# Performance work log

Measured on AMD Instinct MI355X. Metric: run time of the kernel, lower is better.

## Reference

```python
import jax, jax.numpy as jnp
import numpy as np

ANCHOR_NUM = 8
CLASS_NUM = 2
IN_DIM = 1024

def setup_inputs() -> dict:
    key = jax.random.key(0)
    k1, k2, k3, k4 = jax.random.split(key, 4)
    batch_input = jax.random.normal(k1, (64, 512, IN_DIM), dtype=jnp.float32)
    # labels in {-1, 0, 1}: -1 = padding, 0 = negative anchor, 1 = positive anchor
    anchor_labels = jax.random.randint(k2, (64, 512, ANCHOR_NUM), 0, 3, dtype=jnp.int64 if jax.config.read('jax_enable_x64') else jnp.int32) - 1
    lim = 1.0 / np.sqrt(IN_DIM)
    W = jax.random.uniform(k3, (IN_DIM, ANCHOR_NUM * CLASS_NUM), dtype=jnp.float32, minval=-lim, maxval=lim)
    b = jax.random.uniform(k4, (ANCHOR_NUM * CLASS_NUM,), dtype=jnp.float32, minval=-lim, maxval=lim)
    return {"batch_input": batch_input, "W": W, "b": b, "anchor_labels": anchor_labels}

def reference(batch_input, W, b, anchor_labels):
    B, S, _ = batch_input.shape
    # logits: (B, S, anchor_num, class_num)
    logits = (jnp.einsum('bsd,dk->bsk', batch_input, W) + b).reshape(B, S, ANCHOR_NUM, CLASS_NUM)
    predict_label = jnp.argmax(logits, axis=3)  # (B, S, A)
    valid = (anchor_labels != -1)
    labels = jnp.maximum(anchor_labels, 0)  # safe class index for padded entries
    logp = jax.nn.log_softmax(logits, axis=-1)
    nll = -jnp.take_along_axis(logp, labels[..., None].astype(jnp.int32), axis=-1)[..., 0]
    # CrossEntropyLoss (mean) over all non-padding anchors == eval-path gather + CE
    vf = valid.astype(logits.dtype)
    loss = jnp.sum(nll * vf) / jnp.maximum(jnp.sum(vf), 1.0)
    # candidate mask stands in for candidate_idx (positive predictions, non-padding)
    candidate_mask = (predict_label == 1) & valid
    return loss, predict_label, candidate_mask
```

## Files before the change

kernel.cpp:

```cpp
#include <hip/hip_runtime.h>
#include <math.h>


#define ROWS   64
#define NW     8
#define KSLICE 128
#define KCH    16
#define NCH    (KSLICE/KCH)
#define RSTR   136

__global__ __launch_bounds__(512, 2)
void rpn_main(const float* __restrict__ x, const float* __restrict__ W,
              const float* __restrict__ b, const int* __restrict__ lab,
              float* __restrict__ out, float* __restrict__ ws)
{
    __shared__ float red[ROWS * RSTR];

    const int tid  = threadIdx.x;
    const int lane = tid & 63;
    const int ks   = __builtin_amdgcn_readfirstlane(tid >> 6);
    const int row0 = blockIdx.x * ROWS;

    const float* xp = x + (size_t)(row0 + lane) * 1024 + ks * KSLICE;
    const float* wk = W + (size_t)(ks * KSLICE) * 16;

    float acc[16];
#pragma unroll
    for (int c = 0; c < 16; ++c) acc[c] = 0.f;

    float4 pf[4];
#pragma unroll
    for (int j = 0; j < 4; ++j) pf[j] = *(const float4*)(xp + j * 4);

#define FMA16(V, WROW)                                            \
    do {                                                          \
        const float* _w = (WROW);                                 \
        _Pragma("unroll")                                         \
        for (int c = 0; c < 16; ++c)                              \
            acc[c] = fmaf((V), _w[c], acc[c]);                    \
    } while (0)

#pragma unroll 1
    for (int ch = 0; ch < NCH - 1; ++ch) {
        const float* wc = wk + ch * KCH * 16;
        const float* gn = xp + (ch + 1) * KCH;
#pragma unroll
        for (int j = 0; j < 4; ++j) {
            float4 v = pf[j];
            pf[j] = *(const float4*)(gn + j * 4);
            FMA16(v.x, wc + (j * 4 + 0) * 16);
            FMA16(v.y, wc + (j * 4 + 1) * 16);
            FMA16(v.z, wc + (j * 4 + 2) * 16);
            FMA16(v.w, wc + (j * 4 + 3) * 16);
        }
    }
    {
        const float* wc = wk + (NCH - 1) * KCH * 16;
#pragma unroll
        for (int j = 0; j < 4; ++j) {
            float4 v = pf[j];
            FMA16(v.x, wc + (j * 4 + 0) * 16);
            FMA16(v.y, wc + (j * 4 + 1) * 16);
            FMA16(v.z, wc + (j * 4 + 2) * 16);
            FMA16(v.w, wc + (j * 4 + 3) * 16);
        }
    }
#undef FMA16

    __syncthreads();
    {
        float* rp = red + lane * RSTR + ks * 16;
        *(float4*)(rp + 0)  = make_float4(acc[0],  acc[1],  acc[2],  acc[3]);
        *(float4*)(rp + 4)  = make_float4(acc[4],  acc[5],  acc[6],  acc[7]);
        *(float4*)(rp + 8)  = make_float4(acc[8],  acc[9],  acc[10], acc[11]);
        *(float4*)(rp + 12) = make_float4(acc[12], acc[13], acc[14], acc[15]);
    }
    __syncthreads();

    if (tid < ROWS) {
        const int row = row0 + tid;
        float L[16];
#pragma unroll
        for (int c = 0; c < 16; ++c) {
            float s = 0.f;
#pragma unroll
            for (int k = 0; k < NW; ++k) s += red[tid * RSTR + k * 16 + c];
            L[c] = s + b[c];
        }

        const int* labp  = lab + (size_t)row * 8;
        float*     predp = out + 1 + (size_t)row * 8;
        float*     maskp = out + 1 + 262144 + (size_t)row * 8;

        float lsum = 0.f, lcnt = 0.f;
#pragma unroll
        for (int a = 0; a < 8; ++a) {
            float l0 = L[2 * a], l1 = L[2 * a + 1];
            int   lb = labp[a];
            int   pred  = (l1 > l0) ? 1 : 0;
            int   valid = (lb != -1);
            float m   = fmaxf(l0, l1);
            float lse = m + logf(expf(l0 - m) + expf(l1 - m));
            float nll = lse - ((lb == 1) ? l1 : l0);
            if (valid) { lsum += nll; lcnt += 1.f; }
            predp[a] = (float)pred;
            maskp[a] = (pred && valid) ? 1.f : 0.f;
        }

#pragma unroll
        for (int off = 32; off > 0; off >>= 1) {
            lsum += __shfl_down(lsum, off, 64);
            lcnt += __shfl_down(lcnt, off, 64);
        }
        if (tid == 0) {
            atomicAdd(&ws[0], lsum);
            atomicAdd(&ws[1], lcnt);
        }
    }
}

__global__ void rpn_final(const float* __restrict__ ws, float* __restrict__ out)
{
    out[0] = ws[0] / fmaxf(ws[1], 1.f);
}

extern "C" void kernel_launch(void* const* d_in, const int* in_sizes, int n_in,
                              void* d_out, int out_size, void* d_ws, size_t ws_size,
                              hipStream_t stream)
{
    const float* x   = (const float*)d_in[0];
    const float* W   = (const float*)d_in[1];
    const float* b   = (const float*)d_in[2];
    const int*   lab = (const int*)d_in[3];
    float* out = (float*)d_out;
    float* ws  = (float*)d_ws;

    hipMemsetAsync(ws, 0, 2 * sizeof(float), stream);
    rpn_main<<<dim3(512), dim3(512), 0, stream>>>(x, W, b, lab, out, ws);
    rpn_final<<<dim3(1), dim3(1), 0, stream>>>(ws, out);
}
```

Measured before the change: 211.8 us.

## Stage x tiles into LDS via global_load_lds with swizzled layout

```diff
diff --git a/kernel.cpp b/kernel.cpp
--- a/kernel.cpp
+++ b/kernel.cpp
@@ -5,32 +5,46 @@
 #define ROWS   64
 #define NW     8
 #define KSLICE 128
-#define KCH    16
-#define NCH    (KSLICE/KCH)
+#define CHUNK  32
+#define NCH    (KSLICE/CHUNK)
+#define SLABF  (ROWS*CHUNK)
 #define RSTR   136
+
+typedef __attribute__((address_space(3))) void       lds_v;
+typedef const __attribute__((address_space(1))) void gbl_v;
+
+__device__ __forceinline__ void stage16(const float* g, float* l)
+{
+    __builtin_amdgcn_global_load_lds((gbl_v*)g, (lds_v*)l, 16, 0, 0);
+}
 
 __global__ __launch_bounds__(512, 2)
 void rpn_main(const float* __restrict__ x, const float* __restrict__ W,
               const float* __restrict__ b, const int* __restrict__ lab,
               float* __restrict__ out, float* __restrict__ ws)
 {
-    __shared__ float red[ROWS * RSTR];
+    __shared__ float xs[NW * SLABF];
+    float* red = xs;
 
     const int tid  = threadIdx.x;
     const int lane = tid & 63;
     const int ks   = __builtin_amdgcn_readfirstlane(tid >> 6);
     const int row0 = blockIdx.x * ROWS;
 
-    const float* xp = x + (size_t)(row0 + lane) * 1024 + ks * KSLICE;
-    const float* wk = W + (size_t)(ks * KSLICE) * 16;
+    const int rsub = lane >> 3;
+    const int tq   = (lane & 7) ^ rsub;
+
+    float* slab = xs + ks * SLABF;
+    const float* gstage = x + (size_t)(row0 + rsub) * 1024 + ks * KSLICE + tq * 4;
+    const float* wk     = W + (size_t)(ks * KSLICE) * 16;
 
     float acc[16];
 #pragma unroll
     for (int c = 0; c < 16; ++c) acc[c] = 0.f;
 
-    float4 pf[4];
 #pragma unroll
-    for (int j = 0; j < 4; ++j) pf[j] = *(const float4*)(xp + j * 4);
+    for (int i = 0; i < 8; ++i)
+        stage16(gstage + i * 8192, slab + i * 256);
 
 #define FMA16(V, WROW)                                            \
     do {                                                          \
@@ -41,28 +55,31 @@
     } while (0)
 
 #pragma unroll 1
-    for (int ch = 0; ch < NCH - 1; ++ch) {
-        const float* wc = wk + ch * KCH * 16;
-        const float* gn = xp + (ch + 1) * KCH;
+    for (int ch = 0; ch < NCH; ++ch) {
+        asm volatile("s_waitcnt vmcnt(0)" ::: "memory");
+        __builtin_amdgcn_sched_barrier(0);
+
+        float4 xq[8];
 #pragma unroll
-        for (int j = 0; j < 4; ++j) {
-            float4 v = pf[j];
-            pf[j] = *(const float4*)(gn + j * 4);
-            FMA16(v.x, wc + (j * 4 + 0) * 16);
-            FMA16(v.y, wc + (j * 4 + 1) * 16);
-            FMA16(v.z, wc + (j * 4 + 2) * 16);
-            FMA16(v.w, wc + (j * 4 + 3) * 16);
+        for (int t = 0; t < 8; ++t)
+            xq[t] = *(const float4*)(slab + lane * 32 + ((t ^ (lane & 7)) << 2));
+
+        asm volatile("s_waitcnt lgkmcnt(0)" ::: "memory");
+        __builtin_amdgcn_sched_barrier(0);
+        if (ch + 1 < NCH) {
+            const float* g = gstage + (ch + 1) * CHUNK;
+#pragma unroll
+            for (int i = 0; i < 8; ++i)
+                stage16(g + i * 8192, slab + i * 256);
         }
-    }
-    {
-        const float* wc = wk + (NCH - 1) * KCH * 16;
+
+        const float* wc = wk + (size_t)(ch * CHUNK) * 16;
 #pragma unroll
-        for (int j = 0; j < 4; ++j) {
-            float4 v = pf[j];
-            FMA16(v.x, wc + (j * 4 + 0) * 16);
-            FMA16(v.y, wc + (j * 4 + 1) * 16);
-            FMA16(v.z, wc + (j * 4 + 2) * 16);
-            FMA16(v.w, wc + (j * 4 + 3) * 16);
+        for (int t = 0; t < 8; ++t) {
+            FMA16(xq[t].x, wc + (t * 4 + 0) * 16);
+            FMA16(xq[t].y, wc + (t * 4 + 1) * 16);
+            FMA16(xq[t].z, wc + (t * 4 + 2) * 16);
+            FMA16(xq[t].w, wc + (t * 4 + 3) * 16);
         }
     }
 #undef FMA16
```

Result: no change. 215.7 us (+1.9%).

## Split K across two blocks per row tile and move epilogue to final kernel

Applied to the files above, without the earlier changes.

```diff
diff --git a/kernel.cpp b/kernel.cpp
--- a/kernel.cpp
+++ b/kernel.cpp
@@ -4,25 +4,29 @@
 
 #define ROWS   64
 #define NW     8
-#define KSLICE 128
+#define KSL    64
 #define KCH    16
-#define NCH    (KSLICE/KCH)
-#define RSTR   136
+#define NCH    4
+#define RSTR   132
+#define PART_STRIDE (32768u * 16u)
 
-__global__ __launch_bounds__(512, 2)
+__global__ __launch_bounds__(512, 4)
 void rpn_main(const float* __restrict__ x, const float* __restrict__ W,
-              const float* __restrict__ b, const int* __restrict__ lab,
-              float* __restrict__ out, float* __restrict__ ws)
+              float* __restrict__ ws)
 {
     __shared__ float red[ROWS * RSTR];
 
     const int tid  = threadIdx.x;
     const int lane = tid & 63;
-    const int ks   = __builtin_amdgcn_readfirstlane(tid >> 6);
-    const int row0 = blockIdx.x * ROWS;
+    const int wv   = __builtin_amdgcn_readfirstlane(tid >> 6);
+    const int rb   = blockIdx.x & 511;
+    const int kb   = blockIdx.x >> 9;
+    const int row0 = rb * ROWS;
+    const int kse  = (wv + blockIdx.x) & 7;
+    const int chr  = (blockIdx.x >> 3) & 3;
 
-    const float* xp = x + (size_t)(row0 + lane) * 1024 + ks * KSLICE;
-    const float* wk = W + (size_t)(ks * KSLICE) * 16;
+    const float* xp = x + (size_t)(row0 + lane) * 1024 + kb * 512 + kse * KSL;
+    const float* wk = W + (size_t)(kb * 512 + kse * KSL) * 16;
 
     float acc[16];
 #pragma unroll
@@ -30,7 +34,8 @@
 
     float4 pf[4];
 #pragma unroll
-    for (int j = 0; j < 4; ++j) pf[j] = *(const float4*)(xp + j * 4);
+    for (int j = 0; j < 4; ++j)
+        pf[j] = *(const float4*)(xp + chr * KCH + j * 4);
 
 #define FMA16(V, WROW)                                            \
     do {                                                          \
@@ -40,25 +45,16 @@
             acc[c] = fmaf((V), _w[c], acc[c]);                    \
     } while (0)
 
-#pragma unroll 1
-    for (int ch = 0; ch < NCH - 1; ++ch) {
-        const float* wc = wk + ch * KCH * 16;
-        const float* gn = xp + (ch + 1) * KCH;
+#pragma unroll
+    for (int ci = 0; ci < NCH; ++ci) {
+        const int ch  = (ci + chr) & 3;
+        const int chn = (ci + 1 + chr) & 3;
+        const float* wc = wk + ch * (KCH * 16);
 #pragma unroll
         for (int j = 0; j < 4; ++j) {
             float4 v = pf[j];
-            pf[j] = *(const float4*)(gn + j * 4);
-            FMA16(v.x, wc + (j * 4 + 0) * 16);
-            FMA16(v.y, wc + (j * 4 + 1) * 16);
-            FMA16(v.z, wc + (j * 4 + 2) * 16);
-            FMA16(v.w, wc + (j * 4 + 3) * 16);
-        }
-    }
-    {
-        const float* wc = wk + (NCH - 1) * KCH * 16;
-#pragma unroll
-        for (int j = 0; j < 4; ++j) {
-            float4 v = pf[j];
+            if (ci != NCH - 1)
+                pf[j] = *(const float4*)(xp + chn * KCH + j * 4);
             FMA16(v.x, wc + (j * 4 + 0) * 16);
             FMA16(v.y, wc + (j * 4 + 1) * 16);
             FMA16(v.z, wc + (j * 4 + 2) * 16);
@@ -69,7 +65,7 @@
 
     __syncthreads();
     {
-        float* rp = red + lane * RSTR + ks * 16;
+        float* rp = red + lane * RSTR + wv * 16;
         *(float4*)(rp + 0)  = make_float4(acc[0],  acc[1],  acc[2],  acc[3]);
         *(float4*)(rp + 4)  = make_float4(acc[4],  acc[5],  acc[6],  acc[7]);
         *(float4*)(rp + 8)  = make_float4(acc[8],  acc[9],  acc[10], acc[11]);
@@ -77,51 +73,90 @@
     }
     __syncthreads();
 
-    if (tid < ROWS) {
-        const int row = row0 + tid;
-        float L[16];
+    if (tid < 256) {
+        const int row = tid >> 2;
+        const int c0  = (tid & 3) * 4;
+        float4 s = make_float4(0.f, 0.f, 0.f, 0.f);
 #pragma unroll
-        for (int c = 0; c < 16; ++c) {
-            float s = 0.f;
-#pragma unroll
-            for (int k = 0; k < NW; ++k) s += red[tid * RSTR + k * 16 + c];
-            L[c] = s + b[c];
+        for (int k = 0; k < NW; ++k) {
+            float4 t = *(const float4*)(red + row * RSTR + k * 16 + c0);
+            s.x += t.x; s.y += t.y; s.z += t.z; s.w += t.w;
         }
-
-        const int* labp  = lab + (size_t)row * 8;
-        float*     predp = out + 1 + (size_t)row * 8;
-        float*     maskp = out + 1 + 262144 + (size_t)row * 8;
-
-        float lsum = 0.f, lcnt = 0.f;
-#pragma unroll
-        for (int a = 0; a < 8; ++a) {
-            float l0 = L[2 * a], l1 = L[2 * a + 1];
-            int   lb = labp[a];
-            int   pred  = (l1 > l0) ? 1 : 0;
-            int   valid = (lb != -1);
-            float m   = fmaxf(l0, l1);
-            float lse = m + logf(expf(l0 - m) + expf(l1 - m));
-            float nll = lse - ((lb == 1) ? l1 : l0);
-            if (valid) { lsum += nll; lcnt += 1.f; }
-            predp[a] = (float)pred;
-            maskp[a] = (pred && valid) ? 1.f : 0.f;
-        }
-
-#pragma unroll
-        for (int off = 32; off > 0; off >>= 1) {
-            lsum += __shfl_down(lsum, off, 64);
-            lcnt += __shfl_down(lcnt, off, 64);
-        }
-        if (tid == 0) {
-            atomicAdd(&ws[0], lsum);
-            atomicAdd(&ws[1], lcnt);
-        }
+        float* dst = ws + 8 + (size_t)kb * PART_STRIDE
+                   + (size_t)(row0 + row) * 16 + c0;
+        *(float4*)dst = s;
     }
 }
 
-__global__ void rpn_final(const float* __restrict__ ws, float* __restrict__ out)
+__global__ __launch_bounds__(256, 4)
+void rpn_final(const float* __restrict__ b, const int* __restrict__ lab,
+               float* __restrict__ out, float* __restrict__ ws)
 {
-    out[0] = ws[0] / fmaxf(ws[1], 1.f);
+    __shared__ float rsum[8];
+    const int tid = threadIdx.x;
+    const int row = blockIdx.x * 256 + tid;
+
+    const float* p0 = ws + 8 + (size_t)row * 16;
+    const float* p1 = p0 + PART_STRIDE;
+
+    float L[16];
+#pragma unroll
+    for (int q = 0; q < 4; ++q) {
+        float4 a0 = *(const float4*)(p0 + q * 4);
+        float4 a1 = *(const float4*)(p1 + q * 4);
+        L[q * 4 + 0] = a0.x + a1.x + b[q * 4 + 0];
+        L[q * 4 + 1] = a0.y + a1.y + b[q * 4 + 1];
+        L[q * 4 + 2] = a0.z + a1.z + b[q * 4 + 2];
+        L[q * 4 + 3] = a0.w + a1.w + b[q * 4 + 3];
+    }
+
+    const int* labp = lab + (size_t)row * 8;
+    float pv[8], mv[8];
+    float lsum = 0.f, lcnt = 0.f;
+#pragma unroll
+    for (int a = 0; a < 8; ++a) {
+        float l0 = L[2 * a], l1 = L[2 * a + 1];
+        int   lb = labp[a];
+        int   pred  = (l1 > l0) ? 1 : 0;
+        int   valid = (lb != -1);
+        float m   = fmaxf(l0, l1);
+        float lse = m + logf(expf(l0 - m) + expf(l1 - m));
+        float nll = lse - ((lb == 1) ? l1 : l0);
+        if (valid) { lsum += nll; lcnt += 1.f; }
+        pv[a] = (float)pred;
+        mv[a] = (pred && valid) ? 1.f : 0.f;
+    }
+
+    float* predp = out + 1 + (size_t)row * 8;
+    float* maskp = out + 1 + 262144 + (size_t)row * 8;
+    *(float4*)(predp)     = make_float4(pv[0], pv[1], pv[2], pv[3]);
+    *(float4*)(predp + 4) = make_float4(pv[4], pv[5], pv[6], pv[7]);
+    *(float4*)(maskp)     = make_float4(mv[0], mv[1], mv[2], mv[3]);
+    *(float4*)(maskp + 4) = make_float4(mv[4], mv[5], mv[6], mv[7]);
+
+#pragma unroll
+    for (int off = 32; off > 0; off >>= 1) {
+        lsum += __shfl_down(lsum, off, 64);
+        lcnt += __shfl_down(lcnt, off, 64);
+    }
+    if ((tid & 63) == 0) {
+        rsum[(tid >> 6) * 2]     = lsum;
+        rsum[(tid >> 6) * 2 + 1] = lcnt;
+    }
+    __syncthreads();
+    if (tid == 0) {
+        float S = rsum[0] + rsum[2] + rsum[4] + rsum[6];
+        float C = rsum[1] + rsum[3] + rsum[5] + rsum[7];
+        atomicAdd(&ws[0], S);
+        atomicAdd(&ws[1], C);
+        __threadfence();
+        unsigned int old = atomicAdd((unsigned int*)(ws + 2), 1u);
+        if (old == gridDim.x - 1) {
+            float Sf = atomicAdd(&ws[0], 0.f);
+            float Cf = atomicAdd(&ws[1], 0.f);
+            out[0] = Sf / fmaxf(Cf, 1.f);
+        }
+    }
 }
 
 extern "C" void kernel_launch(void* const* d_in, const int* in_sizes, int n_in,
@@ -135,7 +170,7 @@
     float* out = (float*)d_out;
     float* ws  = (float*)d_ws;
 
-    hipMemsetAsync(ws, 0, 2 * sizeof(float), stream);
-    rpn_main<<<dim3(512), dim3(512), 0, stream>>>(x, W, b, lab, out, ws);
-    rpn_final<<<dim3(1), dim3(1), 0, stream>>>(ws, out);
+    hipMemsetAsync(ws, 0, 16, stream);
+    rpn_main<<<dim3(1024), dim3(512), 0, stream>>>(x, W, ws);
+    rpn_final<<<dim3(128), dim3(256), 0, stream>>>(b, lab, out, ws);
 }
```

Result: slower. 219.2 us (+3.5%).
